# Performance work log

Hardware: AMD Instinct MI355X
Metric: run time of the kernel (lower is better)

The kernel has to match this reference:

```python
import math
import jax, jax.numpy as jnp
import numpy as np

H = 12
D_MODEL = 768
D_K = D_MODEL // H
B, S = 2, 2048


def setup_inputs() -> dict:
    key = jax.random.key(0)
    ks = jax.random.split(key, 12)
    sc = 0.02
    inp = {
        "query": jax.random.normal(ks[0], (B, S, D_MODEL), jnp.float32),
        "key": jax.random.normal(ks[1], (B, S, D_MODEL), jnp.float32),
        "value": jax.random.normal(ks[2], (B, S, D_MODEL), jnp.float32),
        # causal mask [B, S, S]: 1 where attendable
        "mask": jnp.broadcast_to(jnp.tril(jnp.ones((S, S), jnp.int32)), (B, S, S)),
        "Wq": sc * jax.random.normal(ks[3], (D_MODEL, D_MODEL), jnp.float32),
        "bq": jnp.zeros((D_MODEL,), jnp.float32),
        "Wk": sc * jax.random.normal(ks[4], (D_MODEL, D_MODEL), jnp.float32),
        "bk": jnp.zeros((D_MODEL,), jnp.float32),
        "Wv": sc * jax.random.normal(ks[5], (D_MODEL, D_MODEL), jnp.float32),
        "bv": jnp.zeros((D_MODEL,), jnp.float32),
        "Wo": sc * jax.random.normal(ks[6], (D_MODEL, D_MODEL), jnp.float32),
        "bo": jnp.zeros((D_MODEL,), jnp.float32),
    }
    return inp


def reference(query, key, value, mask, Wq, bq, Wk, bk, Wv, bv, Wo, bo):
    b, s, _ = query.shape
    # linear projections (torch Linear: x @ W.T + b), split into heads
    def proj(x, W, bias):
        return (x @ W.T + bias).reshape(b, s, H, D_K).transpose(0, 2, 1, 3)  # [B,H,S,Dk]

    q = proj(query, Wq, bq)
    k = proj(key, Wk, bk)
    v = proj(value, Wv, bv)

    scores = jnp.einsum("bhqd,bhkd->bhqk", q, k) / math.sqrt(D_K)  # [B,H,S,S]
    # exponential time-decay bias over key positions 1..S, shape [1,1,1,S]
    time = jnp.exp(-jnp.arange(1, s + 1, dtype=scores.dtype))[None, None, None, :]
    scores = jnp.where(mask[:, None, :, :] == 0, jnp.asarray(-1e9, scores.dtype), scores)
    p_attn = jax.nn.softmax(scores - time, axis=-1)
    x = jnp.einsum("bhqk,bhkd->bhqd", p_attn, v)  # [B,H,S,Dk]
    x = x.transpose(0, 2, 1, 3).reshape(b, s, H * D_K)
    return x @ Wo.T + bo
```

## Files before the change

### kernel.cpp

```cpp
#include <hip/hip_runtime.h>
#include <hip/hip_bf16.h>
#include <math.h>

typedef __bf16 bf16;
typedef __attribute__((ext_vector_type(8))) __bf16 bf16x8;
typedef __attribute__((ext_vector_type(4))) __bf16 bf16x4;
typedef __attribute__((ext_vector_type(4))) float floatx4;

#define NH 12
#define DK 64
#define DM 768
#define NB 2
#define SEQ 2048
#define MTOT (NB * SEQ)
#define WELEM (DM * DM)
#define XELEM (MTOT * DM)

#define QSCALE 0.1803368801111832f
#define LOG2E 1.4426950408889634f

static __device__ __forceinline__ bf16x8 load8(const bf16* p) {
    return *(const bf16x8*)p;
}
static __device__ __forceinline__ float4 ld4(const float* p) {
    return *(const float4*)p;
}
static __device__ __forceinline__ bf16x8 cvt8(const float4 a, const float4 b) {
    bf16x8 r;
    r[0] = (bf16)a.x; r[1] = (bf16)a.y; r[2] = (bf16)a.z; r[3] = (bf16)a.w;
    r[4] = (bf16)b.x; r[5] = (bf16)b.y; r[6] = (bf16)b.z; r[7] = (bf16)b.w;
    return r;
}
static __device__ __forceinline__ float fast_exp2(float x) {
#if __has_builtin(__builtin_amdgcn_exp2f)
    return __builtin_amdgcn_exp2f(x);
#else
    return __expf(x * 0.6931471805599453f);
#endif
}
static __device__ __forceinline__ void async16(const bf16* g, bf16* l) {
    __builtin_amdgcn_global_load_lds((const __attribute__((address_space(1))) void*)g,
                                     (__attribute__((address_space(3))) void*)l,
                                     16, 0, 0);
}

__global__ __launch_bounds__(256) void cvt_kernel(
    const float* __restrict__ wq, const float* __restrict__ wk,
    const float* __restrict__ wv, const float* __restrict__ wo,
    const float* __restrict__ xq, const float* __restrict__ xk, const float* __restrict__ xv,
    bf16* __restrict__ Wb, bf16* __restrict__ Wob,
    bf16* __restrict__ Xqb, bf16* __restrict__ Xkb, bf16* __restrict__ Xvb) {
    const int g = blockIdx.x * 256 + threadIdx.x;
    const int PW = WELEM / 8;
    const int PX = XELEM / 8;
    if (g < 4 * PW) {
        const int wi = g / PW;
        const int rem = g - wi * PW;
        const int n = rem / 96;
        const int t = rem - n * 96;
        const int s = t >> 3;
        const int j = t & 7;
        const float* src = (wi == 0) ? wq : (wi == 1) ? wk : (wi == 2) ? wv : wo;
        bf16* dst = (wi < 3) ? (Wb + (size_t)wi * WELEM) : Wob;
        const float* p = src + (size_t)n * DM + s * 64 + j * 8;
        *(bf16x8*)(dst + (size_t)n * DM + s * 64 + ((j ^ (n & 7)) * 8)) = cvt8(ld4(p), ld4(p + 4));
    } else {
        const int gx = g - 4 * PW;
        const int xi = gx / PX;
        const int rem = gx - xi * PX;
        const int m = rem / 96;
        const int t = rem - m * 96;
        const int s = t >> 3;
        const int j = t & 7;
        const float* src = (xi == 0) ? xq : (xi == 1) ? xk : xv;
        bf16* dst = (xi == 0) ? Xqb : (xi == 1) ? Xkb : Xvb;
        const float* p = src + (size_t)m * DM + s * 64 + j * 8;
        *(bf16x8*)(dst + (size_t)m * DM + s * 64 + ((j ^ (m & 7)) * 8)) = cvt8(ld4(p), ld4(p + 4));
    }
}

__global__ __launch_bounds__(256, 3) void qkv_kernel(
    const bf16* __restrict__ Xqb, const bf16* __restrict__ Xkb, const bf16* __restrict__ Xvb,
    const bf16* __restrict__ Wb,
    const float* __restrict__ bq, const float* __restrict__ bk, const float* __restrict__ bv,
    bf16* __restrict__ Oq, bf16* __restrict__ Ok, bf16* __restrict__ Ov) {
    __shared__ __align__(16) bf16 SM[2 * 64 * 64 + 2 * 128 * 64];
    bf16* As0 = SM;
    bf16* Bs0 = SM + 8192;

    const int tid = threadIdx.x;
    const int id = blockIdx.x;
    const int xcd = id & 7;
    const int sl = id >> 3;
    const int z = sl / 48;
    const int r = sl % 48;
    const int m0 = (xcd * 8 + r / 6) * 64;
    const int n0 = (r % 6) * 128;

    const bf16* X = (z == 0) ? Xqb : (z == 1) ? Xkb : Xvb;
    const bf16* W = Wb + (size_t)z * WELEM;
    const float* bias = (z == 0) ? bq : (z == 1) ? bk : bv;
    bf16* out = (z == 0) ? Oq : (z == 1) ? Ok : Ov;

    const int wv = tid >> 6;
    const int wm = wv >> 1, wn = wv & 1;
    const int lane = tid & 63;
    const int ln = lane & 15;
    const int kq = lane >> 4;
    const int drow = lane >> 3;
    const int dcol = (lane & 7) * 8;

    floatx4 acc[2][4];
#pragma unroll
    for (int i = 0; i < 2; i++)
#pragma unroll
        for (int j = 0; j < 4; j++) acc[i][j] = (floatx4){0.f, 0.f, 0.f, 0.f};

#pragma unroll
    for (int it = 0; it < 2; it++)
        async16(X + (size_t)(m0 + wv * 16 + it * 8 + drow) * DM + dcol,
                As0 + (wv * 16 + it * 8) * 64);
#pragma unroll
    for (int it = 0; it < 4; it++)
        async16(W + (size_t)(n0 + wv * 32 + it * 8 + drow) * DM + dcol,
                Bs0 + (wv * 32 + it * 8) * 64);

    for (int k = 0; k < 12; k++) {
        __syncthreads();
        const bf16* Ap = As0 + (k & 1) * 4096;
        const bf16* Bp = Bs0 + (k & 1) * 8192;
        if (k < 11) {
            const int kc = (k + 1) * 64;
            bf16* An = As0 + ((k + 1) & 1) * 4096;
            bf16* Bn = Bs0 + ((k + 1) & 1) * 8192;
#pragma unroll
            for (int it = 0; it < 2; it++)
                async16(X + (size_t)(m0 + wv * 16 + it * 8 + drow) * DM + kc + dcol,
                        An + (wv * 16 + it * 8) * 64);
#pragma unroll
            for (int it = 0; it < 4; it++)
                async16(W + (size_t)(n0 + wv * 32 + it * 8 + drow) * DM + kc + dcol,
                        Bn + (wv * 32 + it * 8) * 64);
        }
#pragma unroll
        for (int ks = 0; ks < 2; ks++) {
            const int jb = (ks * 4 + kq) ^ (ln & 7);
            bf16x8 af[2], bfm[4];
#pragma unroll
            for (int mt = 0; mt < 2; mt++)
                af[mt] = *(const bf16x8*)&Ap[(wm * 32 + mt * 16 + ln) * 64 + jb * 8];
#pragma unroll
            for (int nt = 0; nt < 4; nt++)
                bfm[nt] = *(const bf16x8*)&Bp[(wn * 64 + nt * 16 + ln) * 64 + jb * 8];
#pragma unroll
            for (int mt = 0; mt < 2; mt++)
#pragma unroll
                for (int nt = 0; nt < 4; nt++)
                    acc[mt][nt] = __builtin_amdgcn_mfma_f32_16x16x32_bf16(af[mt], bfm[nt], acc[mt][nt], 0, 0, 0);
        }
    }

    float bv4[4];
#pragma unroll
    for (int nt = 0; nt < 4; nt++) bv4[nt] = bias[n0 + wn * 64 + nt * 16 + ln];

    if (z < 2) {
        const float qs = (z == 0) ? QSCALE : 1.0f;
        __syncthreads();
        bf16 (*E)[136] = (bf16(*)[136])SM;
#pragma unroll
        for (int mt = 0; mt < 2; mt++)
#pragma unroll
            for (int nt = 0; nt < 4; nt++)
#pragma unroll
                for (int r2 = 0; r2 < 4; r2++)
                    E[wm * 32 + mt * 16 + kq * 4 + r2][wn * 64 + nt * 16 + ln] =
                        (bf16)((acc[mt][nt][r2] + bv4[nt]) * qs);
        __syncthreads();
        const int row = tid >> 2;
        const int cb = (tid & 3) * 32;
        const int m = m0 + row;
        const int b = m >> 11;
        const int s = m & (SEQ - 1);
        const int h = (n0 + cb) >> 6;
        const int d = (n0 + cb) & 63;
        bf16* op = &out[((size_t)(b * NH + h) * SEQ + s) * DK + d];
#pragma unroll
        for (int q2 = 0; q2 < 4; q2++)
            *(bf16x8*)(op + q2 * 8) = *(bf16x8*)&E[row][cb + q2 * 8];
    } else {
        __syncthreads();
        bf16 (*E)[72] = (bf16(*)[72])SM;
#pragma unroll
        for (int nt = 0; nt < 4; nt++)
#pragma unroll
            for (int mt = 0; mt < 2; mt++) {
                bf16x4 v;
#pragma unroll
                for (int r2 = 0; r2 < 4; r2++) v[r2] = (bf16)(acc[mt][nt][r2] + bv4[nt]);
                *(bf16x4*)&E[wn * 64 + nt * 16 + ln][wm * 32 + mt * 16 + kq * 4] = v;
            }
        __syncthreads();
        const int row = tid >> 1;
        const int sc = (tid & 1) * 32;
        const int b = m0 >> 11;
        const int s0 = m0 & (SEQ - 1);
        const int h = (n0 >> 6) + (row >> 6);
        const int d = row & 63;
        bf16* op = &out[(size_t)(b * NH + h) * DK * SEQ + (size_t)d * SEQ + s0 + sc];
#pragma unroll
        for (int q2 = 0; q2 < 4; q2++)
            *(bf16x8*)(op + q2 * 8) = *(bf16x8*)&E[row][sc + q2 * 8];
    }
}


#define VSWZ(g, d) (((g) & 8) | (((g) & 7) ^ ((d) & 7)))

#define QK_BODY(FIRSTC, MASKC)                                                 \
    _Pragma("unroll")                                                          \
    for (int ks = 0; ks < 8; ks++) {                                           \
        const bf16* krow = &Ks[(ks * 16 + ln) << 6];                           \
        const bf16x8 a0 = *(const bf16x8*)&krow[(kq ^ (ln & 7)) * 8];          \
        const bf16x8 a1 = *(const bf16x8*)&krow[((4 + kq) ^ (ln & 7)) * 8];    \
        floatx4 t = (floatx4){0.f, 0.f, 0.f, 0.f};                             \
        t = __builtin_amdgcn_mfma_f32_16x16x32_bf16(a0, qa0, t, 0, 0, 0);      \
        t = __builtin_amdgcn_mfma_f32_16x16x32_bf16(a1, qa1, t, 0, 0, 0);      \
        _Pragma("unroll")                                                      \
        for (int r = 0; r < 4; r++) {                                          \
            float sv = t[r];                                                   \
            if (FIRSTC) {                                                      \
                const int kg = k0 + (ks >> 1) * 32 + (ks & 1) * 4 + kq * 8 + r;\
                sv -= __expf(-(float)(kg + 1)) * LOG2E;                        \
            }                                                                  \
            float pf = fast_exp2(sv);                                          \
            if (MASKC) {                                                       \
                const int kg = k0 + (ks >> 1) * 32 + (ks & 1) * 4 + kq * 8 + r;\
                if (kg > qgl) pf = 0.f;                                        \
            }                                                                  \
            lsum += pf;                                                        \
            pa[ks >> 1][(ks & 1) * 4 + r] = (bf16)pf;                          \
        }                                                                      \
    }

__global__ __launch_bounds__(256) void attn_kernel(const bf16* __restrict__ Q,
                                                   const bf16* __restrict__ K,
                                                   const bf16* __restrict__ Vt,
                                                   bf16* __restrict__ Xout) {
    __shared__ __align__(16) bf16 SM[16384];
    bf16* Ks = SM;
    bf16* Vs = SM + 8192;

    const int tid = threadIdx.x;
    const int wv = tid >> 6;
    const int lane = tid & 63;
    const int ln = lane & 15;
    const int kq = lane >> 4;
    const int krow = tid >> 1;
    const int kprow = (krow & 0x60) | ((krow & 4) << 2) | ((krow & 24) >> 1) | (krow & 3);
    const int kcol = (tid & 1) * 32;
    const int vrow = tid >> 2;
    const int vcol = (tid & 3) * 32;

    const int bidx = blockIdx.x;
    const int rk = (bidx < 256 || bidx >= 512) ? bidx : 767 - bidx;
    const int x = 31 - (rk / 24);
    const int bh = rk % 24;

    const int q0 = x * 64;
    const int qbase = q0 + wv * 16;
    const int nch = (x >> 1) + 1;

    const bf16* Qb = Q + (size_t)bh * SEQ * DK;
    const bf16* Kb = K + (size_t)bh * SEQ * DK;
    const bf16* Vb = Vt + (size_t)bh * SEQ * DK;

    const bf16x8 qa0 = load8(&Qb[(size_t)(qbase + ln) * DK + kq * 8]);
    const bf16x8 qa1 = load8(&Qb[(size_t)(qbase + ln) * DK + 32 + kq * 8]);

    bf16x8 kx[4], vx[4];
#pragma unroll
    for (int q = 0; q < 4; q++) {
        kx[q] = load8(&Kb[(size_t)krow * DK + kcol + q * 8]);
        vx[q] = load8(&Vb[(size_t)vrow * SEQ + vcol + q * 8]);
    }

    float lsum = 0.f;
    floatx4 Oacc[4];
#pragma unroll
    for (int nt = 0; nt < 4; nt++) Oacc[nt] = (floatx4){0.f, 0.f, 0.f, 0.f};

    const int qgl = qbase + ln;

    for (int c = 0; c < nch; c++) {
        const int k0 = c * 128;
        __syncthreads();
#pragma unroll
        for (int q = 0; q < 4; q++) {
            const int jk = (tid & 1) * 4 + q;
            const int jv = (tid & 3) * 4 + q;
            *(bf16x8*)&Ks[(kprow << 6) + ((jk ^ (kprow & 7)) * 8)] = kx[q];
            *(bf16x8*)&Vs[(vrow << 7) + (VSWZ(jv, vrow) * 8)] = vx[q];
        }
        __syncthreads();
        if (c + 1 < nch) {
            const int kn = k0 + 128;
#pragma unroll
            for (int q = 0; q < 4; q++) {
                kx[q] = load8(&Kb[(size_t)(kn + krow) * DK + kcol + q * 8]);
                vx[q] = load8(&Vb[(size_t)vrow * SEQ + kn + vcol + q * 8]);
            }
        }

        bf16x8 pa[4];
        const bool lastc = (c == nch - 1);
        if (c == 0) {
            if (lastc) { QK_BODY(true, true) }
            else       { QK_BODY(true, false) }
        } else if (lastc) {
            QK_BODY(false, true)
        } else {
            QK_BODY(false, false)
        }

        __builtin_amdgcn_s_setprio(1);
#pragma unroll
        for (int nt = 0; nt < 4; nt++) {
            const bf16* vrowp = &Vs[(nt * 16 + ln) << 7];
#pragma unroll
            for (int seg = 0; seg < 4; seg++) {
                const bf16x8 vb = *(const bf16x8*)&vrowp[VSWZ(seg * 4 + kq, ln) * 8];
                Oacc[nt] = __builtin_amdgcn_mfma_f32_16x16x32_bf16(pa[seg], vb, Oacc[nt], 0, 0, 0);
            }
        }
        __builtin_amdgcn_s_setprio(0);
    }

    lsum += __shfl_xor(lsum, 16, 64);
    lsum += __shfl_xor(lsum, 32, 64);
    float rl[4];
#pragma unroll
    for (int r = 0; r < 4; r++) rl[r] = 1.f / __shfl(lsum, kq * 4 + r, 64);

    __syncthreads();
    bf16 (*E)[72] = (bf16(*)[72])SM;
    const int erow = tid >> 2;
    const int ecb = (tid & 3) * 16;
#pragma unroll
    for (int nt = 0; nt < 4; nt++) {
#pragma unroll
        for (int r = 0; r < 4; r++)
            E[wv * 16 + kq * 4 + r][nt * 16 + ln] = (bf16)(Oacc[nt][r] * rl[r]);
    }
    __syncthreads();
    const int b = bh / NH;
    const int h = bh - b * NH;
    const int q = q0 + erow;
    const int j0 = (tid & 3) * 2;
    const int key = erow & 7;
    bf16* rowp = &Xout[((size_t)(b * SEQ + q)) * DM + h * DK];
    *(bf16x8*)(rowp + ((j0 ^ key) * 8)) = *(bf16x8*)&E[erow][ecb];
    *(bf16x8*)(rowp + (((j0 + 1) ^ key) * 8)) = *(bf16x8*)&E[erow][ecb + 8];
}

__global__ __launch_bounds__(256, 3) void outproj_kernel(const bf16* __restrict__ X,
                                                         const bf16* __restrict__ W,
                                                         const float* __restrict__ bias,
                                                         float* __restrict__ out) {
    __shared__ __align__(16) bf16 SM[2 * 64 * 64 + 2 * 128 * 64];
    bf16* As0 = SM;
    bf16* Bs0 = SM + 8192;

    const int tid = threadIdx.x;
    const int id = blockIdx.x;
    const int xcd = id & 7;
    const int sl = id >> 3;
    const int m0 = (xcd * 8 + sl / 6) * 64;
    const int n0 = (sl % 6) * 128;

    const int wv = tid >> 6;
    const int wm = wv >> 1, wn = wv & 1;
    const int lane = tid & 63;
    const int ln = lane & 15;
    const int kq = lane >> 4;
    const int drow = lane >> 3;
    const int dcol = (lane & 7) * 8;

    floatx4 acc[2][4];
#pragma unroll
    for (int i = 0; i < 2; i++)
#pragma unroll
        for (int j = 0; j < 4; j++) acc[i][j] = (floatx4){0.f, 0.f, 0.f, 0.f};

#pragma unroll
    for (int it = 0; it < 2; it++)
        async16(X + (size_t)(m0 + wv * 16 + it * 8 + drow) * DM + dcol,
                As0 + (wv * 16 + it * 8) * 64);
#pragma unroll
    for (int it = 0; it < 4; it++)
        async16(W + (size_t)(n0 + wv * 32 + it * 8 + drow) * DM + dcol,
                Bs0 + (wv * 32 + it * 8) * 64);

    for (int k = 0; k < 12; k++) {
        __syncthreads();
        const bf16* Ap = As0 + (k & 1) * 4096;
        const bf16* Bp = Bs0 + (k & 1) * 8192;
        if (k < 11) {
            const int kc = (k + 1) * 64;
            bf16* An = As0 + ((k + 1) & 1) * 4096;
            bf16* Bn = Bs0 + ((k + 1) & 1) * 8192;
#pragma unroll
            for (int it = 0; it < 2; it++)
                async16(X + (size_t)(m0 + wv * 16 + it * 8 + drow) * DM + kc + dcol,
                        An + (wv * 16 + it * 8) * 64);
#pragma unroll
            for (int it = 0; it < 4; it++)
                async16(W + (size_t)(n0 + wv * 32 + it * 8 + drow) * DM + kc + dcol,
                        Bn + (wv * 32 + it * 8) * 64);
        }
#pragma unroll
        for (int ks = 0; ks < 2; ks++) {
            const int jb = (ks * 4 + kq) ^ (ln & 7);
            bf16x8 af[2], bfm[4];
#pragma unroll
            for (int mt = 0; mt < 2; mt++)
                af[mt] = *(const bf16x8*)&Ap[(wm * 32 + mt * 16 + ln) * 64 + jb * 8];
#pragma unroll
            for (int nt = 0; nt < 4; nt++)
                bfm[nt] = *(const bf16x8*)&Bp[(wn * 64 + nt * 16 + ln) * 64 + jb * 8];
#pragma unroll
            for (int mt = 0; mt < 2; mt++)
#pragma unroll
                for (int nt = 0; nt < 4; nt++)
                    acc[mt][nt] = __builtin_amdgcn_mfma_f32_16x16x32_bf16(af[mt], bfm[nt], acc[mt][nt], 0, 0, 0);
        }
    }

#pragma unroll
    for (int nt = 0; nt < 4; nt++) {
        const int n = n0 + wn * 64 + nt * 16 + ln;
        const float bval = bias[n];
#pragma unroll
        for (int mt = 0; mt < 2; mt++)
#pragma unroll
            for (int r2 = 0; r2 < 4; r2++) {
                const int m = m0 + wm * 32 + mt * 16 + kq * 4 + r2;
                out[(size_t)m * DM + n] = acc[mt][nt][r2] + bval;
            }
    }
}

extern "C" void kernel_launch(void* const* d_in, const int* in_sizes, int n_in,
                              void* d_out, int out_size, void* d_ws, size_t ws_size,
                              hipStream_t stream) {
    const float* query = (const float*)d_in[0];
    const float* key   = (const float*)d_in[1];
    const float* value = (const float*)d_in[2];
    const float* Wq = (const float*)d_in[4];
    const float* bq = (const float*)d_in[5];
    const float* Wk = (const float*)d_in[6];
    const float* bk = (const float*)d_in[7];
    const float* Wv = (const float*)d_in[8];
    const float* bv = (const float*)d_in[9];
    const float* Wo = (const float*)d_in[10];
    const float* bo = (const float*)d_in[11];
    float* out = (float*)d_out;

    bf16* Qws  = (bf16*)d_ws;
    bf16* Kws  = Qws + XELEM;
    bf16* Vtws = Kws + XELEM;
    bf16* Xws  = Vtws + XELEM;
    bf16* Wob  = Xws + XELEM;
    bf16* Xvb  = Wob + WELEM;

    bf16* Wb  = (bf16*)out;
    bf16* Xkb = (bf16*)out + 3 * WELEM;

    bf16* Xqb = Xws;

    const int ncvt = (4 * (WELEM / 8) + 3 * (XELEM / 8)) / 256;
    cvt_kernel<<<ncvt, 256, 0, stream>>>(Wq, Wk, Wv, Wo, query, key, value,
                                         Wb, Wob, Xqb, Xkb, Xvb);

    qkv_kernel<<<1152, 256, 0, stream>>>(Xqb, Xkb, Xvb, Wb, bq, bk, bv,
                                         Qws, Kws, Vtws);

    attn_kernel<<<768, 256, 0, stream>>>(Qws, Kws, Vtws, Xws);

    outproj_kernel<<<384, 256, 0, stream>>>(Xws, Wob, bo, out);
}
```

Baseline: 188.8 us.

## Split attention key range across two blocks and combine partials in new kernel

Each query tile's key chunks are now split between two blocks: one takes the even chunks, the other the odd chunks. Each block writes unnormalized fp32 partial outputs and row sums to workspace. A new combine kernel adds the two partials, normalizes, and writes the bf16 head-interleaved output. This doubles the attention grid to spread the causal workload, at the cost of extra fp32 global traffic and one more kernel launch.

```diff
diff --git a/kernel.cpp b/kernel.cpp
--- a/kernel.cpp
+++ b/kernel.cpp
@@ -246,7 +246,8 @@
 __global__ __launch_bounds__(256) void attn_kernel(const bf16* __restrict__ Q,
                                                    const bf16* __restrict__ K,
                                                    const bf16* __restrict__ Vt,
-                                                   bf16* __restrict__ Xout) {
+                                                   float* __restrict__ Opart,
+                                                   float* __restrict__ Lpart) {
     __shared__ __align__(16) bf16 SM[16384];
     bf16* Ks = SM;
     bf16* Vs = SM + 8192;
@@ -263,9 +264,12 @@
     const int vcol = (tid & 3) * 32;
 
     const int bidx = blockIdx.x;
-    const int rk = (bidx < 256 || bidx >= 512) ? bidx : 767 - bidx;
+    const int pr = bidx >> 1;
+    const int g = bidx & 1;
+    const int rk = (pr < 256 || pr >= 512) ? pr : 767 - pr;
     const int x = 31 - (rk / 24);
     const int bh = rk % 24;
+    const int tile = x * 24 + bh;
 
     const int q0 = x * 64;
     const int qbase = q0 + wv * 16;
@@ -279,10 +283,13 @@
     const bf16x8 qa1 = load8(&Qb[(size_t)(qbase + ln) * DK + 32 + kq * 8]);
 
     bf16x8 kx[4], vx[4];
-#pragma unroll
-    for (int q = 0; q < 4; q++) {
-        kx[q] = load8(&Kb[(size_t)krow * DK + kcol + q * 8]);
-        vx[q] = load8(&Vb[(size_t)vrow * SEQ + vcol + q * 8]);
+    {
+        const int k0i = g * 128;
+#pragma unroll
+        for (int q = 0; q < 4; q++) {
+            kx[q] = load8(&Kb[(size_t)(k0i + krow) * DK + kcol + q * 8]);
+            vx[q] = load8(&Vb[(size_t)vrow * SEQ + k0i + vcol + q * 8]);
+        }
     }
 
     float lsum = 0.f;
@@ -292,7 +299,7 @@
 
     const int qgl = qbase + ln;
 
-    for (int c = 0; c < nch; c++) {
+    for (int c = g; c < nch; c += 2) {
         const int k0 = c * 128;
         __syncthreads();
 #pragma unroll
@@ -303,8 +310,8 @@
             *(bf16x8*)&Vs[(vrow << 7) + (VSWZ(jv, vrow) * 8)] = vx[q];
         }
         __syncthreads();
-        if (c + 1 < nch) {
-            const int kn = k0 + 128;
+        if (c + 2 < nch) {
+            const int kn = k0 + 256;
 #pragma unroll
             for (int q = 0; q < 4; q++) {
                 kx[q] = load8(&Kb[(size_t)(kn + krow) * DK + kcol + q * 8]);
@@ -338,29 +345,62 @@
 
     lsum += __shfl_xor(lsum, 16, 64);
     lsum += __shfl_xor(lsum, 32, 64);
-    float rl[4];
-#pragma unroll
-    for (int r = 0; r < 4; r++) rl[r] = 1.f / __shfl(lsum, kq * 4 + r, 64);
 
     __syncthreads();
-    bf16 (*E)[72] = (bf16(*)[72])SM;
-    const int erow = tid >> 2;
-    const int ecb = (tid & 3) * 16;
+    float* EF = (float*)SM;
+    float* LSs = (float*)SM + 64 * 68;
 #pragma unroll
     for (int nt = 0; nt < 4; nt++) {
 #pragma unroll
         for (int r = 0; r < 4; r++)
-            E[wv * 16 + kq * 4 + r][nt * 16 + ln] = (bf16)(Oacc[nt][r] * rl[r]);
-    }
+            EF[(wv * 16 + kq * 4 + r) * 68 + nt * 16 + ln] = Oacc[nt][r];
+    }
+    if (kq == 0) LSs[wv * 16 + ln] = lsum;
     __syncthreads();
+    float* Obase = Opart + ((size_t)tile * 2 + g) * 4096;
+    const int row = tid >> 2;
+    const int c16 = (tid & 3) * 16;
+#pragma unroll
+    for (int i = 0; i < 4; i++)
+        *(float4*)&Obase[row * 64 + c16 + i * 4] = *(float4*)&EF[row * 68 + c16 + i * 4];
+    if (tid < 64) Lpart[((size_t)tile * 2 + g) * 64 + tid] = LSs[tid];
+}
+
+__global__ __launch_bounds__(256) void combine_kernel(const float* __restrict__ Opart,
+                                                      const float* __restrict__ Lpart,
+                                                      bf16* __restrict__ Xout) {
+    const int tile = blockIdx.x;
+    const int x = tile / 24;
+    const int bh = tile % 24;
+    const int tid = threadIdx.x;
+    const int row = tid >> 2;
+    const int c16 = (tid & 3) * 16;
+
+    const float* O0 = Opart + (size_t)tile * 2 * 4096;
+    const float* O1 = O0 + 4096;
+    const float inv = 1.f / (Lpart[(size_t)tile * 2 * 64 + row] +
+                             Lpart[((size_t)tile * 2 + 1) * 64 + row]);
+
+    const int q = x * 64 + row;
     const int b = bh / NH;
     const int h = bh - b * NH;
-    const int q = q0 + erow;
-    const int j0 = (tid & 3) * 2;
-    const int key = erow & 7;
+    const int key = row & 7;
     bf16* rowp = &Xout[((size_t)(b * SEQ + q)) * DM + h * DK];
-    *(bf16x8*)(rowp + ((j0 ^ key) * 8)) = *(bf16x8*)&E[erow][ecb];
-    *(bf16x8*)(rowp + (((j0 + 1) ^ key) * 8)) = *(bf16x8*)&E[erow][ecb + 8];
+
+#pragma unroll
+    for (int half = 0; half < 2; half++) {
+        const int off = row * 64 + c16 + half * 8;
+        float4 s0 = ld4(&O0[off]);
+        float4 s1 = ld4(&O0[off + 4]);
+        const float4 t0 = ld4(&O1[off]);
+        const float4 t1 = ld4(&O1[off + 4]);
+        s0.x = (s0.x + t0.x) * inv; s0.y = (s0.y + t0.y) * inv;
+        s0.z = (s0.z + t0.z) * inv; s0.w = (s0.w + t0.w) * inv;
+        s1.x = (s1.x + t1.x) * inv; s1.y = (s1.y + t1.y) * inv;
+        s1.z = (s1.z + t1.z) * inv; s1.w = (s1.w + t1.w) * inv;
+        const int j = (tid & 3) * 2 + half;
+        *(bf16x8*)(rowp + ((j ^ key) * 8)) = cvt8(s0, s1);
+    }
 }
 
 __global__ __launch_bounds__(256, 3) void outproj_kernel(const bf16* __restrict__ X,
@@ -472,6 +512,8 @@
     bf16* Xws  = Vtws + XELEM;
     bf16* Wob  = Xws + XELEM;
     bf16* Xvb  = Wob + WELEM;
+    float* Opart = (float*)(Xvb + XELEM);
+    float* Lpart = Opart + (size_t)768 * 2 * 4096;
 
     bf16* Wb  = (bf16*)out;
     bf16* Xkb = (bf16*)out + 3 * WELEM;
@@ -485,7 +527,9 @@
     qkv_kernel<<<1152, 256, 0, stream>>>(Xqb, Xkb, Xvb, Wb, bq, bk, bv,
                                          Qws, Kws, Vtws);
 
-    attn_kernel<<<768, 256, 0, stream>>>(Qws, Kws, Vtws, Xws);
+    attn_kernel<<<1536, 256, 0, stream>>>(Qws, Kws, Vtws, Opart, Lpart);
+
+    combine_kernel<<<768, 256, 0, stream>>>(Opart, Lpart, Xws);
 
     outproj_kernel<<<384, 256, 0, stream>>>(Xws, Wob, bo, out);
 }
```

Result: slower. 196.4 us (+4.0%).
